# Optimization experiments

Hardware: AMD Instinct MI355X
Metric: run time of the kernel (lower is better)

The kernel has to match this reference:

```python
import jax, jax.numpy as jnp
import numpy as np

V, D, C = 50257, 1024, 131072  # vocab size, hidden dim, cache length
SMOOTH = 32.0  # kernel bandwidth (scaled up from 0.2 to avoid exp overflow at d=1024)


def setup_inputs() -> dict:
    key = jax.random.key(0)
    k1, k2, k3 = jax.random.split(key, 3)
    h_t = jax.random.normal(k1, (V, D), dtype=jnp.float32)
    cache_h = jax.random.normal(k2, (C, D), dtype=jnp.float32)
    cache_words = jax.random.randint(k3, (C,), 0, V)
    return {"h_t": h_t, "cache_h": cache_h, "cache_words": cache_words}


def reference(h_t, cache_h, cache_words):
    # Original: for each vocab id v, sum over cache elems (w_i, h_i) with w_i == v
    # of exp(||h_i - h_t[v]|| / smooth), then log_softmax over vocab.
    # Vectorized: gather the query hidden for each cache element, compute the
    # per-element kernel value, and scatter-add (segment_sum) by vocab id.
    q = h_t[cache_words]                                   # [C, D] gather
    dist = jnp.sqrt(jnp.sum((cache_h - q) ** 2, axis=-1))  # [C] euclidean norms
    vals = jnp.exp(dist / SMOOTH)                          # [C] kernel weights
    cache_p = jax.ops.segment_sum(vals, cache_words, num_segments=h_t.shape[0])  # [V]
    return jax.nn.log_softmax(cache_p[None, :], axis=-1)   # [1, V]
```

## Files before the change

kernel.cpp:

```cpp
#include <hip/hip_runtime.h>
#include <math.h>

#define V 50257
#define D 1024
#define C 131072
#define SMOOTH 32.0f

typedef float fx4 __attribute__((ext_vector_type(4)));

__global__ __launch_bounds__(256) void k_scatter(
    const float* __restrict__ h_t,
    const float* __restrict__ cache_h,
    const int* __restrict__ cache_words,
    float* __restrict__ p)
{
    const int wave = threadIdx.x >> 6;
    const int lane = threadIdx.x & 63;
    const int i = (blockIdx.x << 2) + wave;

    const int w = cache_words[i];
    const fx4* ch = (const fx4*)(cache_h + (size_t)i * D);
    const fx4* ht = (const fx4*)(h_t + (size_t)w * D);

    float ssq = 0.0f;
#pragma unroll
    for (int k = 0; k < 4; ++k) {
        fx4 a = __builtin_nontemporal_load(&ch[lane + (k << 6)]);
        fx4 b = ht[lane + (k << 6)];
        fx4 d = a - b;
        ssq += d.x * d.x + d.y * d.y + d.z * d.z + d.w * d.w;
    }
#pragma unroll
    for (int off = 32; off > 0; off >>= 1)
        ssq += __shfl_xor(ssq, off, 64);

    if (lane == 0) {
        float val = expf(sqrtf(ssq) * (1.0f / SMOOTH));
        atomicAdd(&p[w], val);
    }
}

__global__ __launch_bounds__(256) void k_max(
    const float* __restrict__ p, unsigned int* __restrict__ m)
{
    float lm = 0.0f;
    for (int v = blockIdx.x * blockDim.x + threadIdx.x; v < V;
         v += gridDim.x * blockDim.x)
        lm = fmaxf(lm, p[v]);
#pragma unroll
    for (int off = 32; off > 0; off >>= 1)
        lm = fmaxf(lm, __shfl_xor(lm, off, 64));
    __shared__ float s[4];
    if ((threadIdx.x & 63) == 0) s[threadIdx.x >> 6] = lm;
    __syncthreads();
    if (threadIdx.x == 0) {
        lm = fmaxf(fmaxf(s[0], s[1]), fmaxf(s[2], s[3]));
        atomicMax(m, __float_as_uint(lm));
    }
}

__global__ __launch_bounds__(256) void k_sumexp(
    const float* __restrict__ p, const unsigned int* __restrict__ m,
    float* __restrict__ S)
{
    const float mm = __uint_as_float(*m);
    float ls = 0.0f;
    for (int v = blockIdx.x * blockDim.x + threadIdx.x; v < V;
         v += gridDim.x * blockDim.x)
        ls += expf(p[v] - mm);
#pragma unroll
    for (int off = 32; off > 0; off >>= 1)
        ls += __shfl_xor(ls, off, 64);
    __shared__ float s[4];
    if ((threadIdx.x & 63) == 0) s[threadIdx.x >> 6] = ls;
    __syncthreads();
    if (threadIdx.x == 0)
        atomicAdd(S, s[0] + s[1] + s[2] + s[3]);
}

__global__ __launch_bounds__(256) void k_finalize(
    const float* __restrict__ p, const unsigned int* __restrict__ m,
    const float* __restrict__ S, float* __restrict__ out)
{
    const float shift = __uint_as_float(*m) + logf(*S);
    for (int v = blockIdx.x * blockDim.x + threadIdx.x; v < V;
         v += gridDim.x * blockDim.x)
        out[v] = p[v] - shift;
}

extern "C" void kernel_launch(void* const* d_in, const int* in_sizes, int n_in,
                              void* d_out, int out_size, void* d_ws, size_t ws_size,
                              hipStream_t stream)
{
    const float* h_t         = (const float*)d_in[0];
    const float* cache_h     = (const float*)d_in[1];
    const int*   cache_words = (const int*)d_in[2];
    float* out = (float*)d_out;

    float*        p = (float*)d_ws;
    unsigned int* m = (unsigned int*)((char*)d_ws + (size_t)V * sizeof(float));
    float*        S = (float*)((char*)d_ws + (size_t)V * sizeof(float) + sizeof(unsigned int));

    (void)hipMemsetAsync(d_ws, 0, (size_t)V * sizeof(float) + 2 * sizeof(unsigned int), stream);

    k_scatter<<<C / 4, 256, 0, stream>>>(h_t, cache_h, cache_words, p);

    k_max     <<<99, 256, 0, stream>>>(p, m);
    k_sumexp  <<<99, 256, 0, stream>>>(p, m, S);
    k_finalize<<<99, 256, 0, stream>>>(p, m, S, out);
}
```

Before: 805.4 us.

## Process two cache rows per wave and fuse log-softmax into one block

The scatter kernel now handles two cache rows per wavefront, interleaving their loads to raise memory-level parallelism, and launches half as many blocks. The three log-softmax kernels (max, sum-exp, finalize) become one single-block kernel of 1024 threads with shared-memory reductions. This removes two launches and the global atomics for max and sum. The cost is that the softmax stage runs on a single CU.

```diff
diff --git a/kernel.cpp b/kernel.cpp
--- a/kernel.cpp
+++ b/kernel.cpp
@@ -16,76 +16,77 @@
 {
     const int wave = threadIdx.x >> 6;
     const int lane = threadIdx.x & 63;
-    const int i = (blockIdx.x << 2) + wave;
+    const int i0 = (blockIdx.x << 3) + (wave << 1);
+    const int i1 = i0 + 1;
 
-    const int w = cache_words[i];
-    const fx4* ch = (const fx4*)(cache_h + (size_t)i * D);
-    const fx4* ht = (const fx4*)(h_t + (size_t)w * D);
+    const int w0 = cache_words[i0];
+    const int w1 = cache_words[i1];
+    const fx4* ch0 = (const fx4*)(cache_h + (size_t)i0 * D);
+    const fx4* ch1 = (const fx4*)(cache_h + (size_t)i1 * D);
+    const fx4* ht0 = (const fx4*)(h_t + (size_t)w0 * D);
+    const fx4* ht1 = (const fx4*)(h_t + (size_t)w1 * D);
 
-    float ssq = 0.0f;
+    float ssq0 = 0.0f, ssq1 = 0.0f;
 #pragma unroll
     for (int k = 0; k < 4; ++k) {
-        fx4 a = __builtin_nontemporal_load(&ch[lane + (k << 6)]);
-        fx4 b = ht[lane + (k << 6)];
-        fx4 d = a - b;
-        ssq += d.x * d.x + d.y * d.y + d.z * d.z + d.w * d.w;
+        fx4 a0 = __builtin_nontemporal_load(&ch0[lane + (k << 6)]);
+        fx4 b0 = ht0[lane + (k << 6)];
+        fx4 a1 = __builtin_nontemporal_load(&ch1[lane + (k << 6)]);
+        fx4 b1 = ht1[lane + (k << 6)];
+        fx4 d0 = a0 - b0;
+        fx4 d1 = a1 - b1;
+        ssq0 += d0.x * d0.x + d0.y * d0.y + d0.z * d0.z + d0.w * d0.w;
+        ssq1 += d1.x * d1.x + d1.y * d1.y + d1.z * d1.z + d1.w * d1.w;
     }
 #pragma unroll
-    for (int off = 32; off > 0; off >>= 1)
-        ssq += __shfl_xor(ssq, off, 64);
-
-    if (lane == 0) {
-        float val = expf(sqrtf(ssq) * (1.0f / SMOOTH));
-        atomicAdd(&p[w], val);
+    for (int off = 32; off > 0; off >>= 1) {
+        ssq0 += __shfl_xor(ssq0, off, 64);
+        ssq1 += __shfl_xor(ssq1, off, 64);
     }
+    if (lane == 0)
+        atomicAdd(&p[w0], expf(sqrtf(ssq0) * (1.0f / SMOOTH)));
+    if (lane == 32)
+        atomicAdd(&p[w1], expf(sqrtf(ssq1) * (1.0f / SMOOTH)));
 }
 
-__global__ __launch_bounds__(256) void k_max(
-    const float* __restrict__ p, unsigned int* __restrict__ m)
+__global__ __launch_bounds__(1024) void k_logsoftmax(
+    const float* __restrict__ p, float* __restrict__ out)
 {
+    __shared__ float red[16];
+    __shared__ float bcast;
+    const int tid = threadIdx.x;
+
     float lm = 0.0f;
-    for (int v = blockIdx.x * blockDim.x + threadIdx.x; v < V;
-         v += gridDim.x * blockDim.x)
-        lm = fmaxf(lm, p[v]);
+    for (int v = tid; v < V; v += 1024) lm = fmaxf(lm, p[v]);
 #pragma unroll
     for (int off = 32; off > 0; off >>= 1)
         lm = fmaxf(lm, __shfl_xor(lm, off, 64));
-    __shared__ float s[4];
-    if ((threadIdx.x & 63) == 0) s[threadIdx.x >> 6] = lm;
+    if ((tid & 63) == 0) red[tid >> 6] = lm;
     __syncthreads();
-    if (threadIdx.x == 0) {
-        lm = fmaxf(fmaxf(s[0], s[1]), fmaxf(s[2], s[3]));
-        atomicMax(m, __float_as_uint(lm));
+    if (tid == 0) {
+        float mm = red[0];
+        for (int k = 1; k < 16; ++k) mm = fmaxf(mm, red[k]);
+        bcast = mm;
     }
-}
+    __syncthreads();
+    const float m = bcast;
 
-__global__ __launch_bounds__(256) void k_sumexp(
-    const float* __restrict__ p, const unsigned int* __restrict__ m,
-    float* __restrict__ S)
-{
-    const float mm = __uint_as_float(*m);
     float ls = 0.0f;
-    for (int v = blockIdx.x * blockDim.x + threadIdx.x; v < V;
-         v += gridDim.x * blockDim.x)
-        ls += expf(p[v] - mm);
+    for (int v = tid; v < V; v += 1024) ls += expf(p[v] - m);
 #pragma unroll
     for (int off = 32; off > 0; off >>= 1)
         ls += __shfl_xor(ls, off, 64);
-    __shared__ float s[4];
-    if ((threadIdx.x & 63) == 0) s[threadIdx.x >> 6] = ls;
+    if ((tid & 63) == 0) red[tid >> 6] = ls;
     __syncthreads();
-    if (threadIdx.x == 0)
-        atomicAdd(S, s[0] + s[1] + s[2] + s[3]);
-}
+    if (tid == 0) {
+        float S = 0.0f;
+        for (int k = 0; k < 16; ++k) S += red[k];
+        bcast = m + logf(S);
+    }
+    __syncthreads();
+    const float shift = bcast;
 
-__global__ __launch_bounds__(256) void k_finalize(
-    const float* __restrict__ p, const unsigned int* __restrict__ m,
-    const float* __restrict__ S, float* __restrict__ out)
-{
-    const float shift = __uint_as_float(*m) + logf(*S);
-    for (int v = blockIdx.x * blockDim.x + threadIdx.x; v < V;
-         v += gridDim.x * blockDim.x)
-        out[v] = p[v] - shift;
+    for (int v = tid; v < V; v += 1024) out[v] = p[v] - shift;
 }
 
 extern "C" void kernel_launch(void* const* d_in, const int* in_sizes, int n_in,
@@ -97,15 +98,11 @@
     const int*   cache_words = (const int*)d_in[2];
     float* out = (float*)d_out;
 
-    float*        p = (float*)d_ws;
-    unsigned int* m = (unsigned int*)((char*)d_ws + (size_t)V * sizeof(float));
-    float*        S = (float*)((char*)d_ws + (size_t)V * sizeof(float) + sizeof(unsigned int));
+    float* p = (float*)d_ws;
 
-    (void)hipMemsetAsync(d_ws, 0, (size_t)V * sizeof(float) + 2 * sizeof(unsigned int), stream);
+    (void)hipMemsetAsync(p, 0, (size_t)V * sizeof(float), stream);
 
-    k_scatter<<<C / 4, 256, 0, stream>>>(h_t, cache_h, cache_words, p);
+    k_scatter<<<C / 8, 256, 0, stream>>>(h_t, cache_h, cache_words, p);
 
-    k_max     <<<99, 256, 0, stream>>>(p, m);
-    k_sumexp  <<<99, 256, 0, stream>>>(p, m, S);
-    k_finalize<<<99, 256, 0, stream>>>(p, m, S, out);
+    k_logsoftmax<<<1, 1024, 0, stream>>>(p, out);
 }
```

Measured after the change: 823.6 us. 1.02x slower.
